# Kernel optimization log

Measured on AMD Instinct MI355X. Metric: run time of the kernel, lower is better.

The kernel has to match this reference:

```python
import jax, jax.numpy as jnp
import numpy as np

# Static module configuration (matches init_kwargs)
B, CIN, COUT, K, H, W = 4, 32, 32, 3, 128, 128
UM = 2                      # um_dim: 2D vector fields
NW = ((K - 1) // 2) * 4     # num_weights = radius*4 = 4


def setup_inputs() -> dict:
    key = jax.random.key(0)
    k1, k2, k3 = jax.random.split(key, 3)
    params = jax.random.normal(k1, (COUT, CIN, NW, 4), jnp.float32)
    basis = jax.random.normal(k2, (NW, 4, K, K, UM, UM), jnp.float32)
    # Replicate the init-time scaling of the torch module:
    # std over the (non-zero) outer-product kernel, then scale params and basis.
    init_kernel = jnp.einsum('abcd,cdefgh->abcdefgh', params, basis)
    stds = jnp.std(init_kernel)  # random basis -> all entries nonzero
    scaler = jnp.sqrt(0.6 / (np.sqrt(CIN) * (K ** 2) * stds))
    params = params * scaler
    basis = basis * scaler
    bias_term = jnp.ones((1, COUT, 2, 1, 1), jnp.float32) / 100.0
    b = jnp.float32(0.01)
    xx = jax.random.normal(k3, (B, CIN * UM, H, W), jnp.float32)
    return {'xx': xx, 'params': params, 'basis': basis,
            'bias_term': bias_term, 'b': b}


def _forward(xx, params, basis, bias_term, b):
    Bn, C, Hh, Ww = xx.shape
    I, O = CIN, COUT
    # --- get_kernel: einsum + transposes -> conv weight (O*2, I*2, K, K) ---
    Kr = jnp.einsum('abcd,cdefgh->abefgh', params, basis)      # (O,I,K,K,2,2)
    kernel = jnp.transpose(Kr, (0, 4, 1, 5, 2, 3)).reshape(O * 2, I * 2, K, K)
    # --- unfold with replicate padding: P[b,c,kh,kw,h,w] ---
    xp = jnp.pad(xx, ((0, 0), (0, 0), (1, 1), (1, 1)), mode='edge')
    P = jnp.stack([xp[:, :, i:i + Hh, j:j + Ww]
                   for i in range(K) for j in range(K)], axis=2)
    P = P.reshape(Bn, C, K, K, Hh, Ww)
    # --- per-window mean subtraction over (input_channels, kh, kw) ---
    P5 = P.reshape(Bn, I, UM, K, K, Hh, Ww)
    avgs = P5.mean(axis=(1, 3, 4), keepdims=True)              # (B,1,2,1,1,H,W)
    P = (P5 - avgs).reshape(Bn, C, K, K, Hh, Ww)
    avgs = avgs[:, :, :, 0, 0]                                 # (B,1,2,H,W)
    # --- strided conv2d on the blown-up grid == this einsum:
    # big[b,c,3h+di,3w+dj] = P[b,c,kh=dj,kw=di,h,w], so kernel (di,dj)=(p,q)
    # pairs with patch (kh=q, kw=p).
    out = jnp.einsum('bcqphw,ocpq->bohw', P, kernel)           # (B,O*2,H,W)
    out = out.reshape(Bn, O, 2, Hh, Ww) + bias_term
    # --- 'relu' vector activation: normalize, zero where norm <= b ---
    norm = jnp.sqrt(out[:, :, 0] ** 2 + out[:, :, 1] ** 2)[:, :, None]
    out = jnp.where(norm - b <= 0.0, 0.0, out / norm)
    # --- add_mean ---
    out = out + avgs
    return out.reshape(Bn, O * 2, Hh, Ww)


def reference(xx, params, basis, bias_term, b):
    return _forward(xx, params, basis, bias_term, b)
```

## Files before the change

kernel.cpp:

```cpp
#include <hip/hip_runtime.h>

#define BN 4
#define CH 64
#define HH 128
#define WW 128
#define PIX (HH*WW)

#define OFF_WL  0
#define OFF_S   36864
#define OFF_AVG 36992

__device__ __forceinline__ int iclamp(int v, int lo, int hi) {
    return v < lo ? lo : (v > hi ? hi : v);
}

__global__ __launch_bounds__(256) void k_prep(const float* __restrict__ params,
                                              const float* __restrict__ basis,
                                              const float* __restrict__ x,
                                              float* __restrict__ Wl,
                                              float* __restrict__ S,
                                              float* __restrict__ avg) {
    int bx = blockIdx.x;
    if (bx < 144) {
        int idx = bx * 256 + threadIdx.x;
        int oc  = idx & 63;
        int tap = (idx >> 6) % 9;
        int c   = idx / 576;
        int q = tap / 3, p = tap % 3;
        int o = oc >> 1, g = oc & 1;
        int i = c >> 1, u = c & 1;
        float s = 0.f;
        #pragma unroll
        for (int n = 0; n < 4; ++n)
            #pragma unroll
            for (int d = 0; d < 4; ++d)
                s = fmaf(params[((o * 32 + i) * 4 + n) * 4 + d],
                         basis[((((n * 4 + d) * 3 + p) * 3 + q) * 2 + g) * 2 + u], s);
        Wl[idx] = s;
    } else if (bx == 144) {
        int t = threadIdx.x;
        if (t < 128) {
            int u = t >> 6, oc = t & 63;
            int o = oc >> 1, g = oc & 1;
            float s = 0.f;
            #pragma unroll
            for (int nd = 0; nd < 16; ++nd) {
                int n = nd >> 2, d = nd & 3;
                float pa = 0.f;
                for (int i = 0; i < 32; ++i)
                    pa += params[((o * 32 + i) * 4 + n) * 4 + d];
                float sb = 0.f;
                #pragma unroll
                for (int e = 0; e < 3; ++e)
                    #pragma unroll
                    for (int f = 0; f < 3; ++f)
                        sb += basis[((((n * 4 + d) * 3 + e) * 3 + f) * 2 + g) * 2 + u];
                s = fmaf(pa, sb, s);
            }
            S[t] = s;
        }
    } else {
        int id = bx - 145;
        int tile = id & 63;
        int u    = (id >> 6) & 1;
        int b    = id >> 7;
        int ty0 = (tile >> 3) * 16, tx0 = (tile & 7) * 16;

        __shared__ float hs[18][19];
        int t = threadIdx.x;
        for (int cell = t; cell < 324; cell += 256) {
            int hy = cell / 18, hx = cell - (cell / 18) * 18;
            int gy = iclamp(ty0 + hy - 1, 0, HH - 1);
            int gx = iclamp(tx0 + hx - 1, 0, WW - 1);
            const float* xp = x + ((size_t)b * CH + u) * PIX + gy * WW + gx;
            float s = 0.f;
            #pragma unroll
            for (int i = 0; i < 32; ++i) s += xp[(size_t)i * 2 * PIX];
            hs[hy][hx] = s;
        }
        __syncthreads();
        int py = t >> 4, px = t & 15;
        float s = hs[py][px]     + hs[py][px + 1]     + hs[py][px + 2]
                + hs[py + 1][px] + hs[py + 1][px + 1] + hs[py + 1][px + 2]
                + hs[py + 2][px] + hs[py + 2][px + 1] + hs[py + 2][px + 2];
        avg[(size_t)(b * 2 + u) * PIX + (ty0 + py) * WW + (tx0 + px)] = s * (1.0f / 288.0f);
    }
}

__global__ __launch_bounds__(256, 8) void k_main(
    const float* __restrict__ x,
    const float* __restrict__ Wl,
    const float* __restrict__ S,
    const float* __restrict__ bias,
    const float* __restrict__ avg,
    const float* __restrict__ bptr,
    float* __restrict__ out)
{
    int tile   = blockIdx.x;
    int ocbase = blockIdx.y * 8;
    int b      = blockIdx.z;
    int ty = threadIdx.x >> 4, tx = threadIdx.x & 15;
    int h = (tile >> 3) * 16 + ty;
    int w = (tile & 7) * 16 + tx;

    int hm = h > 0 ? h - 1 : 0, hp = h < HH - 1 ? h + 1 : HH - 1;
    int wm = w > 0 ? w - 1 : 0, wp = w < WW - 1 ? w + 1 : WW - 1;
    int rowoff[3] = { hm * WW, h * WW, hp * WW };
    int coloff[3] = { wm, w, wp };
    int off[9];
    #pragma unroll
    for (int r = 0; r < 3; ++r)
        #pragma unroll
        for (int p = 0; p < 3; ++p)
            off[r * 3 + p] = rowoff[r] + coloff[p];

    float acc[8];
    #pragma unroll
    for (int j = 0; j < 8; ++j) acc[j] = 0.f;

    const float* xc = x + (size_t)b * CH * PIX;
    const float* wc = Wl + ocbase;

    float xv[9];
    #pragma unroll
    for (int k = 0; k < 9; ++k) xv[k] = xc[off[k]];

    for (int c = 0; c < CH; ++c) {
        const float* xn = xc + (c < CH - 1 ? PIX : 0);
        float xf[9];
        #pragma unroll
        for (int k = 0; k < 9; ++k) xf[k] = xn[off[k]];

        #pragma unroll
        for (int t = 0; t < 9; ++t) {
            const float* wt = wc + t * 64;
            float xt = xv[t];
            #pragma unroll
            for (int j = 0; j < 8; ++j)
                acc[j] = fmaf(xt, wt[j], acc[j]);
        }
        #pragma unroll
        for (int k = 0; k < 9; ++k) xv[k] = xf[k];
        xc += PIX;
        wc += 576;
    }

    int pix = h * WW + w;
    float a0 = avg[(size_t)(b * 2 + 0) * PIX + pix];
    float a1 = avg[(size_t)(b * 2 + 1) * PIX + pix];
    float bthr = bptr[0];

    float* ob = out + (size_t)b * CH * PIX + pix;
    #pragma unroll
    for (int j = 0; j < 8; j += 2) {
        int oc = ocbase + j;
        float t0 = acc[j]     - a0 * S[oc]     - a1 * S[64 + oc]     + bias[oc];
        float t1 = acc[j + 1] - a0 * S[oc + 1] - a1 * S[64 + oc + 1] + bias[oc + 1];
        float n = sqrtf(t0 * t0 + t1 * t1);
        float r0, r1;
        if (n - bthr <= 0.f) { r0 = 0.f; r1 = 0.f; }
        else { r0 = t0 / n; r1 = t1 / n; }
        ob[(size_t)oc * PIX]       = r0 + a0;
        ob[(size_t)(oc + 1) * PIX] = r1 + a1;
    }
}

extern "C" void kernel_launch(void* const* d_in, const int* in_sizes, int n_in,
                              void* d_out, int out_size, void* d_ws, size_t ws_size,
                              hipStream_t stream) {
    const float* xx     = (const float*)d_in[0];
    const float* params = (const float*)d_in[1];
    const float* basis  = (const float*)d_in[2];
    const float* bias   = (const float*)d_in[3];
    const float* bptr   = (const float*)d_in[4];
    float* out = (float*)d_out;
    float* ws  = (float*)d_ws;

    float* Wl  = ws + OFF_WL;
    float* S   = ws + OFF_S;
    float* avg = ws + OFF_AVG;

    k_prep<<<657, 256, 0, stream>>>(params, basis, xx, Wl, S, avg);

    dim3 grid(64, 8, BN);
    k_main<<<grid, 256, 0, stream>>>(xx, Wl, S, bias, avg, bptr, out);
}
```

Before: 171.1 us.

## Stage input halo tiles in shared memory and regroup weights per output group

The main kernel now loads an 18x18 halo tile for 8 channels at a time into LDS and reads its 3x3 neighbourhoods from there, instead of issuing 9 global loads per channel per thread. Weights are rewritten in the prep kernel into a layout contiguous per 8-output-channel group, so each block reads one linear stretch. This trades the register prefetch pipeline for block-wide barriers and about 10KB of LDS per block, which may lower occupancy.

```diff
diff --git a/kernel.cpp b/kernel.cpp
--- a/kernel.cpp
+++ b/kernel.cpp
@@ -36,7 +36,7 @@
             for (int d = 0; d < 4; ++d)
                 s = fmaf(params[((o * 32 + i) * 4 + n) * 4 + d],
                          basis[((((n * 4 + d) * 3 + p) * 3 + q) * 2 + g) * 2 + u], s);
-        Wl[idx] = s;
+        Wl[(((oc >> 3) * 64 + c) * 9 + tap) * 8 + (oc & 7)] = s;
     } else if (bx == 144) {
         int t = threadIdx.x;
         if (t < 128) {
@@ -96,53 +96,52 @@
     const float* __restrict__ bptr,
     float* __restrict__ out)
 {
-    int tile   = blockIdx.x;
-    int ocbase = blockIdx.y * 8;
-    int b      = blockIdx.z;
+    __shared__ float sm[8][18][18];
+
+    int tile = blockIdx.x;
+    int ocg  = blockIdx.y;
+    int b    = blockIdx.z;
     int ty = threadIdx.x >> 4, tx = threadIdx.x & 15;
-    int h = (tile >> 3) * 16 + ty;
-    int w = (tile & 7) * 16 + tx;
-
-    int hm = h > 0 ? h - 1 : 0, hp = h < HH - 1 ? h + 1 : HH - 1;
-    int wm = w > 0 ? w - 1 : 0, wp = w < WW - 1 ? w + 1 : WW - 1;
-    int rowoff[3] = { hm * WW, h * WW, hp * WW };
-    int coloff[3] = { wm, w, wp };
-    int off[9];
-    #pragma unroll
-    for (int r = 0; r < 3; ++r)
-        #pragma unroll
-        for (int p = 0; p < 3; ++p)
-            off[r * 3 + p] = rowoff[r] + coloff[p];
+    int h0 = (tile >> 3) * 16, w0 = (tile & 7) * 16;
+    int h = h0 + ty, w = w0 + tx;
 
     float acc[8];
     #pragma unroll
     for (int j = 0; j < 8; ++j) acc[j] = 0.f;
 
-    const float* xc = x + (size_t)b * CH * PIX;
-    const float* wc = Wl + ocbase;
+    const float* xb = x + (size_t)b * CH * PIX;
+    const float* wbase = Wl + (size_t)ocg * 64 * 72;
 
-    float xv[9];
-    #pragma unroll
-    for (int k = 0; k < 9; ++k) xv[k] = xc[off[k]];
+    for (int c0 = 0; c0 < CH; c0 += 8) {
+        __syncthreads();
+        for (int cell = threadIdx.x; cell < 8 * 324; cell += 256) {
+            int cc = cell / 324;
+            int r  = cell - cc * 324;
+            int hy = r / 18, hx = r - (r / 18) * 18;
+            int gy = iclamp(h0 - 1 + hy, 0, HH - 1);
+            int gx = iclamp(w0 - 1 + hx, 0, WW - 1);
+            sm[cc][hy][hx] = xb[(size_t)(c0 + cc) * PIX + gy * WW + gx];
+        }
+        __syncthreads();
 
-    for (int c = 0; c < CH; ++c) {
-        const float* xn = xc + (c < CH - 1 ? PIX : 0);
-        float xf[9];
+        const float* wc = wbase + c0 * 72;
         #pragma unroll
-        for (int k = 0; k < 9; ++k) xf[k] = xn[off[k]];
-
-        #pragma unroll
-        for (int t = 0; t < 9; ++t) {
-            const float* wt = wc + t * 64;
-            float xt = xv[t];
+        for (int cc = 0; cc < 8; ++cc) {
+            float xv[9];
             #pragma unroll
-            for (int j = 0; j < 8; ++j)
-                acc[j] = fmaf(xt, wt[j], acc[j]);
+            for (int dy = 0; dy < 3; ++dy)
+                #pragma unroll
+                for (int dx = 0; dx < 3; ++dx)
+                    xv[dy * 3 + dx] = sm[cc][ty + dy][tx + dx];
+            const float* wt = wc + cc * 72;
+            #pragma unroll
+            for (int t = 0; t < 9; ++t) {
+                float xt = xv[t];
+                #pragma unroll
+                for (int j = 0; j < 8; ++j)
+                    acc[j] = fmaf(xt, wt[t * 8 + j], acc[j]);
+            }
         }
-        #pragma unroll
-        for (int k = 0; k < 9; ++k) xv[k] = xf[k];
-        xc += PIX;
-        wc += 576;
     }
 
     int pix = h * WW + w;
@@ -153,7 +152,7 @@
     float* ob = out + (size_t)b * CH * PIX + pix;
     #pragma unroll
     for (int j = 0; j < 8; j += 2) {
-        int oc = ocbase + j;
+        int oc = ocg * 8 + j;
         float t0 = acc[j]     - a0 * S[oc]     - a1 * S[64 + oc]     + bias[oc];
         float t1 = acc[j + 1] - a0 * S[oc + 1] - a1 * S[64 + oc + 1] + bias[oc + 1];
         float n = sqrtf(t0 * t0 + t1 * t1);
```

Measured after the change: 174.0 us. Within noise of the previous version (+1.7%).
